# Kernel tuning notes

Measured on AMD Instinct MI355X. Metric: run time of the kernel, lower is better.

The kernel has to match this reference:

```python
import jax, jax.numpy as jnp
import numpy as np

B, Dx, Dz, Dy, H = 4096, 512, 512, 256, 2048
T0, T1 = 0.0, 1.0
N_STEPS = 64


def setup_inputs() -> dict:
    key = jax.random.key(0)
    ks = jax.random.split(key, 9)
    X = jax.random.normal(ks[0], (B, Dx), jnp.float32)
    # P sampled Uniform(0.01, 0.1) as in the torch module
    P = jax.random.uniform(ks[1], (Dz, Dx), jnp.float32, 0.01, 0.1)
    # A scaled so spectral radius ~1 -> exp(A*T) stays bounded over the integration
    A = jax.random.normal(ks[2], (Dz, Dz), jnp.float32) * (Dz ** -0.5)
    W1 = jax.random.normal(ks[3], (H, Dz), jnp.float32) * (Dz ** -0.5)
    b1 = jax.random.normal(ks[4], (H,), jnp.float32) * 0.01
    W2 = jax.random.normal(ks[5], (H, H), jnp.float32) * (H ** -0.5)
    b2 = jax.random.normal(ks[6], (H,), jnp.float32) * 0.01
    W3 = jax.random.normal(ks[7], (Dy, H), jnp.float32) * (H ** -0.5)
    b3 = jax.random.normal(ks[8], (Dy,), jnp.float32) * 0.01
    return dict(X=X, P=P, A=A, W1=W1, b1=b1, W2=W2, b2=b2, W3=W3, b3=b3,
                n_steps=N_STEPS)


def reference(X, P, A, W1, b1, W2, b2, W3, b3, n_steps):
    # Z0 = einsum('ji,bi->bj', P, X)  -> projection into latent ODE state
    z0 = X @ P.T  # [B, Dz]
    dt = jnp.float32((T1 - T0) / n_steps)

    def f(z):  # dz/dt = A z, batched: einsum('ji,bi->bj', A, z)
        return z @ A.T

    def rk4_step(z, _):
        k1 = f(z)
        k2 = f(z + 0.5 * dt * k1)
        k3 = f(z + 0.5 * dt * k2)
        k4 = f(z + dt * k3)
        return z + (dt / 6.0) * (k1 + 2.0 * k2 + 2.0 * k3 + k4), None

    zT, _ = jax.lax.scan(rk4_step, z0, None, length=n_steps)  # [B, Dz]

    # QnnMatrixODE MLP head (n_layers=3): Lin+ReLU, Lin+ReLU, Lin
    h = jax.nn.relu(zT @ W1.T + b1)
    h = jax.nn.relu(h @ W2.T + b2)
    y = h @ W3.T + b3  # [B, Dy]
    return y
```

## Files before the change

kernel.cpp:

```cpp
#include <hip/hip_runtime.h>

#define BDIM 4096
#define DX 512
#define DZ 512
#define DY 256
#define HD 2048
#define NSTEPS 64
#define LDT 72

typedef __attribute__((ext_vector_type(8))) short bf16x8;
typedef __attribute__((ext_vector_type(4))) float f32x4;

__device__ inline unsigned short f2bf(float f) {
    unsigned u = __float_as_uint(f);
    unsigned r = 0x7FFFu + ((u >> 16) & 1u);
    return (unsigned short)((u + r) >> 16);
}
__device__ inline float bf2f(unsigned short h) {
    return __uint_as_float(((unsigned)h) << 16);
}

#define GLDS16(g, l)                                                            \
    __builtin_amdgcn_global_load_lds((const __attribute__((address_space(1))) void*)(g), \
                                     (__attribute__((address_space(3))) void*)(l), 16, 0, 0)

struct CvtJobs {
    const float* src[5];
    unsigned short* hi[5];
    unsigned short* lo[5];
    int n4[5];
};
__global__ __launch_bounds__(256) void cvt_multi_k(CvtJobs J) {
    const int j = blockIdx.y;
    const int i4 = blockIdx.x * 256 + threadIdx.x;
    if (i4 >= J.n4[j]) return;
    float4 v = ((const float4*)J.src[j])[i4];
    ushort4 h;
    h.x = f2bf(v.x); h.y = f2bf(v.y); h.z = f2bf(v.z); h.w = f2bf(v.w);
    ((ushort4*)J.hi[j])[i4] = h;
    if (J.lo[j]) {
        ushort4 l;
        l.x = f2bf(v.x - bf2f(h.x));
        l.y = f2bf(v.y - bf2f(h.y));
        l.z = f2bf(v.z - bf2f(h.z));
        l.w = f2bf(v.w - bf2f(h.w));
        ((ushort4*)J.lo[j])[i4] = l;
    }
}

__global__ __launch_bounds__(256) void split_t_k(const float* __restrict__ A0,
                                                 unsigned short* __restrict__ H0,
                                                 unsigned short* __restrict__ L0,
                                                 const float* __restrict__ A1,
                                                 unsigned short* __restrict__ H1,
                                                 unsigned short* __restrict__ L1, int D) {
    const float* A = blockIdx.z ? A1 : A0;
    unsigned short* HT = blockIdx.z ? H1 : H0;
    unsigned short* LT = blockIdx.z ? L1 : L0;
    __shared__ float t[32][33];
    const int bx = blockIdx.x * 32, by = blockIdx.y * 32;
    const int x = threadIdx.x, y = threadIdx.y;
#pragma unroll
    for (int dy = 0; dy < 32; dy += 8)
        t[y + dy][x] = A[(size_t)(by + y + dy) * D + bx + x];
    __syncthreads();
#pragma unroll
    for (int dy = 0; dy < 32; dy += 8) {
        float v = t[x][y + dy];
        unsigned short h = f2bf(v);
        size_t o = (size_t)(bx + y + dy) * D + by + x;
        HT[o] = h;
        LT[o] = f2bf(v - bf2f(h));
    }
}

__global__ __launch_bounds__(256) void taylor_t_k(const float* __restrict__ Am,
                                                  const float* __restrict__ M2f,
                                                  const float* __restrict__ M3f,
                                                  const float* __restrict__ M4f,
                                                  unsigned short* __restrict__ Sh,
                                                  unsigned short* __restrict__ Sl,
                                                  unsigned short* __restrict__ STh,
                                                  unsigned short* __restrict__ STl,
                                                  int D, float h) {
    __shared__ float t[32][33];
    const float c2 = 0.5f * h * h;
    const float c3 = h * h * h * (1.0f / 6.0f);
    const float c4 = h * h * h * h * (1.0f / 24.0f);
    const int bx = blockIdx.x * 32, by = blockIdx.y * 32;
    const int x = threadIdx.x, y = threadIdx.y;
#pragma unroll
    for (int dy = 0; dy < 32; dy += 8) {
        const int row = by + y + dy, col = bx + x;
        const size_t idx = (size_t)row * D + col;
        float s = h * Am[idx] + c2 * M2f[idx] + c3 * M3f[idx] + c4 * M4f[idx];
        if (row == col) s += 1.0f;
        t[y + dy][x] = s;
        unsigned short hi = f2bf(s);
        Sh[idx] = hi;
        Sl[idx] = f2bf(s - bf2f(hi));
    }
    __syncthreads();
#pragma unroll
    for (int dy = 0; dy < 32; dy += 8) {
        float s = t[x][y + dy];
        size_t o = (size_t)(bx + y + dy) * D + by + x;
        unsigned short hi = f2bf(s);
        STh[o] = hi;
        STl[o] = f2bf(s - bf2f(hi));
    }
}

struct G64In { const unsigned short *Ahi, *Alo, *Bhi, *Blo; };
struct G64Out { float* Cf32; unsigned short *Chi, *Clo, *CThi, *CTlo; };

__device__ __forceinline__ void g64_core(int bx, int by, int M, int N, int K,
                                         G64In in, G64Out o,
                                         unsigned short* Ash, unsigned short* Asl,
                                         unsigned short* Bsh, unsigned short* Bsl) {
    const int tid = threadIdx.x;
    const int lane = tid & 63;
    const int wave = tid >> 6;
    const int wr = wave >> 1, wc = wave & 1;
    const int row0 = by * 64, col0 = bx * 64;
    const int sr = tid >> 2;
    const int sk = (tid & 3) * 16;

    const int niter = K >> 6;
    bf16x8 pa0, pa1, pl0, pl1, pb0, pb1, pq0, pq1;
    {
        const unsigned short* ar = in.Ahi + (size_t)(row0 + sr) * K + sk;
        const unsigned short* al = in.Alo + (size_t)(row0 + sr) * K + sk;
        const unsigned short* br = in.Bhi + (size_t)(col0 + sr) * K + sk;
        const unsigned short* bl = in.Blo + (size_t)(col0 + sr) * K + sk;
        pa0 = *(const bf16x8*)ar; pa1 = *(const bf16x8*)(ar + 8);
        pl0 = *(const bf16x8*)al; pl1 = *(const bf16x8*)(al + 8);
        pb0 = *(const bf16x8*)br; pb1 = *(const bf16x8*)(br + 8);
        pq0 = *(const bf16x8*)bl; pq1 = *(const bf16x8*)(bl + 8);
    }

    f32x4 acc[4] = {};
    const int mb = wr * 32 + (lane & 15);
    const int nb = wc * 32 + (lane & 15);

    for (int it = 0; it < niter; ++it) {
        __syncthreads();
        *(bf16x8*)&Ash[sr * LDT + sk] = pa0; *(bf16x8*)&Ash[sr * LDT + sk + 8] = pa1;
        *(bf16x8*)&Asl[sr * LDT + sk] = pl0; *(bf16x8*)&Asl[sr * LDT + sk + 8] = pl1;
        *(bf16x8*)&Bsh[sr * LDT + sk] = pb0; *(bf16x8*)&Bsh[sr * LDT + sk + 8] = pb1;
        *(bf16x8*)&Bsl[sr * LDT + sk] = pq0; *(bf16x8*)&Bsl[sr * LDT + sk + 8] = pq1;
        __syncthreads();

        {
            const int kn = (it + 1 < niter) ? ((it + 1) << 6) : 0;
            const unsigned short* ar = in.Ahi + (size_t)(row0 + sr) * K + kn + sk;
            const unsigned short* al = in.Alo + (size_t)(row0 + sr) * K + kn + sk;
            const unsigned short* br = in.Bhi + (size_t)(col0 + sr) * K + kn + sk;
            const unsigned short* bl = in.Blo + (size_t)(col0 + sr) * K + kn + sk;
            pa0 = *(const bf16x8*)ar; pa1 = *(const bf16x8*)(ar + 8);
            pl0 = *(const bf16x8*)al; pl1 = *(const bf16x8*)(al + 8);
            pb0 = *(const bf16x8*)br; pb1 = *(const bf16x8*)(br + 8);
            pq0 = *(const bf16x8*)bl; pq1 = *(const bf16x8*)(bl + 8);
        }

#pragma unroll
        for (int kh = 0; kh < 2; ++kh) {
            const int kk = kh * 32 + (lane >> 4) * 8;
            bf16x8 ah[2], alx[2], bh[2], blx[2];
#pragma unroll
            for (int t = 0; t < 2; ++t) {
                ah[t]  = *(const bf16x8*)&Ash[(mb + t * 16) * LDT + kk];
                alx[t] = *(const bf16x8*)&Asl[(mb + t * 16) * LDT + kk];
                bh[t]  = *(const bf16x8*)&Bsh[(nb + t * 16) * LDT + kk];
                blx[t] = *(const bf16x8*)&Bsl[(nb + t * 16) * LDT + kk];
            }
#pragma unroll
            for (int mt = 0; mt < 2; ++mt)
#pragma unroll
                for (int nt = 0; nt < 2; ++nt) {
                    acc[mt * 2 + nt] = __builtin_amdgcn_mfma_f32_16x16x32_bf16(
                        ah[mt], bh[nt], acc[mt * 2 + nt], 0, 0, 0);
                    acc[mt * 2 + nt] = __builtin_amdgcn_mfma_f32_16x16x32_bf16(
                        ah[mt], blx[nt], acc[mt * 2 + nt], 0, 0, 0);
                    acc[mt * 2 + nt] = __builtin_amdgcn_mfma_f32_16x16x32_bf16(
                        alx[mt], bh[nt], acc[mt * 2 + nt], 0, 0, 0);
                }
        }
    }

#pragma unroll
    for (int mt = 0; mt < 2; ++mt) {
        const int grow = row0 + wr * 32 + mt * 16 + (lane >> 4) * 4;
#pragma unroll
        for (int nt = 0; nt < 2; ++nt) {
            const int gcol = col0 + wc * 32 + nt * 16 + (lane & 15);
            f32x4 a = acc[mt * 2 + nt];
            unsigned short h4[4], l4[4];
#pragma unroll
            for (int i = 0; i < 4; ++i) {
                h4[i] = f2bf(a[i]);
                l4[i] = f2bf(a[i] - bf2f(h4[i]));
            }
            if (o.Cf32) {
#pragma unroll
                for (int i = 0; i < 4; ++i) o.Cf32[(size_t)(grow + i) * N + gcol] = a[i];
            }
            if (o.Chi) {
#pragma unroll
                for (int i = 0; i < 4; ++i) o.Chi[(size_t)(grow + i) * N + gcol] = h4[i];
            }
            if (o.Clo) {
#pragma unroll
                for (int i = 0; i < 4; ++i) o.Clo[(size_t)(grow + i) * N + gcol] = l4[i];
            }
            if (o.CThi) {
                ushort4 u = {h4[0], h4[1], h4[2], h4[3]};
                *(ushort4*)&o.CThi[(size_t)gcol * M + grow] = u;
            }
            if (o.CTlo) {
                ushort4 u = {l4[0], l4[1], l4[2], l4[3]};
                *(ushort4*)&o.CTlo[(size_t)gcol * M + grow] = u;
            }
        }
    }
}

__global__ __launch_bounds__(256) void g64_one(G64In in, G64Out o, int M, int N, int K) {
    __shared__ unsigned short Ash[64 * LDT], Asl[64 * LDT], Bsh[64 * LDT], Bsl[64 * LDT];
    g64_core(blockIdx.x, blockIdx.y, M, N, K, in, o, Ash, Asl, Bsh, Bsl);
}

__global__ __launch_bounds__(256) void g64_dual(G64In i0, G64Out o0, G64In i1, G64Out o1,
                                                int M, int N, int K) {
    __shared__ unsigned short Ash[64 * LDT], Asl[64 * LDT], Bsh[64 * LDT], Bsl[64 * LDT];
    g64_core(blockIdx.x, blockIdx.y, M, N, K, blockIdx.z ? i1 : i0, blockIdx.z ? o1 : o0,
             Ash, Asl, Bsh, Bsl);
}

template <int RELU, int BIAS, int OUT_BF16>
__global__ __launch_bounds__(256) void gemm_bf16(int M, int N, int K,
                                                 const unsigned short* __restrict__ A,
                                                 const unsigned short* __restrict__ B,
                                                 void* __restrict__ C,
                                                 const float* __restrict__ bias) {
    __shared__ unsigned short As[128 * 32];
    __shared__ unsigned short Bs[128 * 32];

    const int tid = threadIdx.x;
    const int lane = tid & 63;
    const int wave = tid >> 6;
    const int wr = wave >> 1, wc = wave & 1;
    const int row0 = blockIdx.y * 128;
    const int col0 = blockIdx.x * 128;

    const int srow = lane >> 2;
    const int schunk = (lane & 3) * 8;

    f32x4 acc[4][4] = {};

    for (int k0 = 0; k0 < K; k0 += 32) {
        const int r0 = wave * 32;
        GLDS16(A + (size_t)(row0 + r0 + srow) * K + k0 + schunk, &As[r0 * 32]);
        GLDS16(A + (size_t)(row0 + r0 + 16 + srow) * K + k0 + schunk, &As[(r0 + 16) * 32]);
        GLDS16(B + (size_t)(col0 + r0 + srow) * K + k0 + schunk, &Bs[r0 * 32]);
        GLDS16(B + (size_t)(col0 + r0 + 16 + srow) * K + k0 + schunk, &Bs[(r0 + 16) * 32]);
        __syncthreads();

        const int kk = (lane >> 4) * 8;
        const int mbase = wr * 64 + (lane & 15);
        const int nbase = wc * 64 + (lane & 15);
        bf16x8 af[4], bf[4];
#pragma unroll
        for (int t = 0; t < 4; ++t) {
            af[t] = *(const bf16x8*)&As[(mbase + t * 16) * 32 + kk];
            bf[t] = *(const bf16x8*)&Bs[(nbase + t * 16) * 32 + kk];
        }
#pragma unroll
        for (int mt = 0; mt < 4; ++mt)
#pragma unroll
            for (int nt = 0; nt < 4; ++nt)
                acc[mt][nt] = __builtin_amdgcn_mfma_f32_16x16x32_bf16(af[mt], bf[nt],
                                                                      acc[mt][nt], 0, 0, 0);
        __syncthreads();
    }

#pragma unroll
    for (int mt = 0; mt < 4; ++mt) {
        const int grow = row0 + wr * 64 + mt * 16 + (lane >> 4) * 4;
#pragma unroll
        for (int nt = 0; nt < 4; ++nt) {
            const int gcol = col0 + wc * 64 + nt * 16 + (lane & 15);
            const float bv = BIAS ? bias[gcol] : 0.0f;
#pragma unroll
            for (int i = 0; i < 4; ++i) {
                float v = acc[mt][nt][i] + bv;
                if (RELU) v = fmaxf(v, 0.0f);
                const size_t off = (size_t)(grow + i) * N + gcol;
                if (OUT_BF16)
                    ((unsigned short*)C)[off] = f2bf(v);
                else
                    ((float*)C)[off] = v;
            }
        }
    }
}

__global__ __launch_bounds__(256) void gemm64nt_f32(int M, int N, int K,
                                                    const unsigned short* __restrict__ A,
                                                    const unsigned short* __restrict__ B,
                                                    float* __restrict__ C,
                                                    const float* __restrict__ bias) {
    __shared__ unsigned short As[64 * 32];
    __shared__ unsigned short Bs[64 * 32];
    const int tid = threadIdx.x;
    const int lane = tid & 63;
    const int wave = tid >> 6;
    const int wr = wave >> 1, wc = wave & 1;
    const int row0 = blockIdx.y * 64;
    const int col0 = blockIdx.x * 64;
    const int r = tid >> 2, kq = (tid & 3) * 8;

    f32x4 acc[4] = {};

    for (int k0 = 0; k0 < K; k0 += 32) {
        bf16x8 av = *(const bf16x8*)(A + (size_t)(row0 + r) * K + k0 + kq);
        bf16x8 bv = *(const bf16x8*)(B + (size_t)(col0 + r) * K + k0 + kq);
        __syncthreads();
        *(bf16x8*)&As[r * 32 + kq] = av;
        *(bf16x8*)&Bs[r * 32 + kq] = bv;
        __syncthreads();

        const int kk = (lane >> 4) * 8;
        const int mb = wr * 32 + (lane & 15);
        const int nb = wc * 32 + (lane & 15);
        bf16x8 af[2], bf[2];
#pragma unroll
        for (int t = 0; t < 2; ++t) {
            af[t] = *(const bf16x8*)&As[(mb + t * 16) * 32 + kk];
            bf[t] = *(const bf16x8*)&Bs[(nb + t * 16) * 32 + kk];
        }
#pragma unroll
        for (int mt = 0; mt < 2; ++mt)
#pragma unroll
            for (int nt = 0; nt < 2; ++nt)
                acc[mt * 2 + nt] = __builtin_amdgcn_mfma_f32_16x16x32_bf16(
                    af[mt], bf[nt], acc[mt * 2 + nt], 0, 0, 0);
    }

#pragma unroll
    for (int mt = 0; mt < 2; ++mt) {
        const int grow = row0 + wr * 32 + mt * 16 + (lane >> 4) * 4;
#pragma unroll
        for (int nt = 0; nt < 2; ++nt) {
            const int gcol = col0 + wc * 32 + nt * 16 + (lane & 15);
            const float bv = bias ? bias[gcol] : 0.0f;
#pragma unroll
            for (int i = 0; i < 4; ++i)
                C[(size_t)(grow + i) * N + gcol] = acc[mt * 2 + nt][i] + bv;
        }
    }
}

extern "C" void kernel_launch(void* const* d_in, const int* in_sizes, int n_in,
                              void* d_out, int out_size, void* d_ws, size_t ws_size,
                              hipStream_t stream) {
    const float* X  = (const float*)d_in[0];
    const float* P  = (const float*)d_in[1];
    const float* Am = (const float*)d_in[2];
    const float* W1 = (const float*)d_in[3];
    const float* b1 = (const float*)d_in[4];
    const float* W2 = (const float*)d_in[5];
    const float* b2 = (const float*)d_in[6];
    const float* W3 = (const float*)d_in[7];
    const float* b3 = (const float*)d_in[8];
    float* out = (float*)d_out;

    const float h = 1.0f / (float)NSTEPS;
    const size_t S = (size_t)DZ * DZ;

    char* p = (char*)d_ws;
    auto alloc_f = [&](size_t n) { float* r = (float*)p; p += n * 4; return r; };
    auto alloc_h = [&](size_t n) { unsigned short* r = (unsigned short*)p; p += ((n * 2 + 15) & ~15ull); return r; };
    unsigned short* Xb   = alloc_h((size_t)BDIM * DX);
    unsigned short* W2b  = alloc_h((size_t)HD * HD);
    unsigned short* W3b  = alloc_h((size_t)DY * HD);
    unsigned short* W1h  = alloc_h((size_t)HD * DZ);
    unsigned short* W1l  = alloc_h((size_t)HD * DZ);
    unsigned short* Ah   = alloc_h(S);
    unsigned short* Al   = alloc_h(S);
    unsigned short* ATh  = alloc_h(S);
    unsigned short* ATl  = alloc_h(S);
    unsigned short* PTh  = alloc_h(S);
    unsigned short* PTl  = alloc_h(S);
    float* M2f = alloc_f(S);
    float* M3f = alloc_f(S);
    float* M4f = alloc_f(S);
    unsigned short* M2h  = alloc_h(S);
    unsigned short* M2l  = alloc_h(S);
    unsigned short* M2Th = alloc_h(S);
    unsigned short* M2Tl = alloc_h(S);
    unsigned short* Shb[2]  = {alloc_h(S), alloc_h(S)};
    unsigned short* Slb[2]  = {alloc_h(S), alloc_h(S)};
    unsigned short* SThb[2] = {alloc_h(S), alloc_h(S)};
    unsigned short* STlb[2] = {alloc_h(S), alloc_h(S)};
    unsigned short* RTh  = alloc_h(S);
    unsigned short* RTl  = alloc_h(S);
    unsigned short* C1b  = alloc_h((size_t)HD * DZ);
    unsigned short* h1b  = alloc_h((size_t)BDIM * HD);
    unsigned short* h2b  = alloc_h((size_t)BDIM * HD);

    CvtJobs J;
    J.src[0] = X;  J.hi[0] = Xb;  J.lo[0] = nullptr; J.n4[0] = BDIM * DX / 4;
    J.src[1] = W2; J.hi[1] = W2b; J.lo[1] = nullptr; J.n4[1] = HD * HD / 4;
    J.src[2] = W3; J.hi[2] = W3b; J.lo[2] = nullptr; J.n4[2] = DY * HD / 4;
    J.src[3] = W1; J.hi[3] = W1h; J.lo[3] = W1l;     J.n4[3] = HD * DZ / 4;
    J.src[4] = Am; J.hi[4] = Ah;  J.lo[4] = Al;      J.n4[4] = (int)(S / 4);
    cvt_multi_k<<<dim3(HD * HD / 4 / 256, 5), 256, 0, stream>>>(J);

    split_t_k<<<dim3(DZ / 32, DZ / 32, 2), dim3(32, 8), 0, stream>>>(
        Am, ATh, ATl, P, PTh, PTl, DZ);

    dim3 g8(DZ / 64, DZ / 64);
    const G64Out ONULL = {nullptr, nullptr, nullptr, nullptr, nullptr};

    {
        G64In i{Ah, Al, ATh, ATl};
        G64Out o{M2f, M2h, M2l, M2Th, M2Tl};
        g64_one<<<g8, 256, 0, stream>>>(i, o, DZ, DZ, DZ);
    }
    {
        G64In i0{M2h, M2l, ATh, ATl};
        G64Out o0 = ONULL; o0.Cf32 = M3f;
        G64In i1{M2h, M2l, M2Th, M2Tl};
        G64Out o1 = ONULL; o1.Cf32 = M4f;
        g64_dual<<<dim3(DZ / 64, DZ / 64, 2), 256, 0, stream>>>(i0, o0, i1, o1, DZ, DZ, DZ);
    }
    taylor_t_k<<<dim3(DZ / 32, DZ / 32), dim3(32, 8), 0, stream>>>(
        Am, M2f, M3f, M4f, Shb[0], Slb[0], SThb[0], STlb[0], DZ, h);
    int cur = 0;
    for (int s = 0; s < 6; ++s) {
        G64In i{Shb[cur], Slb[cur], SThb[cur], STlb[cur]};
        G64Out o{nullptr, Shb[1 - cur], Slb[1 - cur], SThb[1 - cur], STlb[1 - cur]};
        g64_one<<<g8, 256, 0, stream>>>(i, o, DZ, DZ, DZ);
        cur ^= 1;
    }
    {
        G64In i{Shb[cur], Slb[cur], PTh, PTl};
        G64Out o = ONULL; o.CThi = RTh; o.CTlo = RTl;
        g64_one<<<g8, 256, 0, stream>>>(i, o, DZ, DZ, DZ);
    }
    {
        G64In i{W1h, W1l, RTh, RTl};
        G64Out o = ONULL; o.Chi = C1b;
        g64_one<<<dim3(DZ / 64, HD / 64), 256, 0, stream>>>(i, o, HD, DZ, DZ);
    }

    gemm_bf16<1, 1, 1><<<dim3(HD / 128, BDIM / 128), 256, 0, stream>>>(
        BDIM, HD, DX, Xb, C1b, h1b, b1);
    gemm_bf16<1, 1, 1><<<dim3(HD / 128, BDIM / 128), 256, 0, stream>>>(
        BDIM, HD, HD, h1b, W2b, h2b, b2);
    gemm64nt_f32<<<dim3(DY / 64, BDIM / 64), 256, 0, stream>>>(
        BDIM, DY, HD, h2b, W3b, out, b3);
}
```

Before: 303.4 us.

## Compute exp(A) via Horner Taylor series and retile the MLP GEMMs

The matrix exponential is no longer built as an RK4 step matrix raised to the 64th power by six squarings. It is now a degree-15 Taylor series of exp(A) evaluated in Horner form on A^4, with the low-order polynomial blocks formed in one elementwise kernel and added in the GEMM epilogue. This replaces the Taylor build and six squarings with three Horner GEMMs, so there are fewer dependent 512x512 launches. The MLP GEMMs change as well: the first two use 64x128 tiles, which doubles the block count, and the last layer gets a double-buffered K=64 loop with register prefetch and padded LDS. The exact exponential differs slightly from the RK4 result, within its truncation error.

```diff
diff --git a/kernel.cpp b/kernel.cpp
--- a/kernel.cpp
+++ b/kernel.cpp
@@ -5,7 +5,6 @@
 #define DZ 512
 #define DY 256
 #define HD 2048
-#define NSTEPS 64
 #define LDT 72
 
 typedef __attribute__((ext_vector_type(8))) short bf16x8;
@@ -74,44 +73,50 @@
     }
 }
 
-__global__ __launch_bounds__(256) void taylor_t_k(const float* __restrict__ Am,
-                                                  const float* __restrict__ M2f,
-                                                  const float* __restrict__ M3f,
-                                                  const float* __restrict__ M4f,
-                                                  unsigned short* __restrict__ Sh,
-                                                  unsigned short* __restrict__ Sl,
-                                                  unsigned short* __restrict__ STh,
-                                                  unsigned short* __restrict__ STl,
-                                                  int D, float h) {
-    __shared__ float t[32][33];
-    const float c2 = 0.5f * h * h;
-    const float c3 = h * h * h * (1.0f / 6.0f);
-    const float c4 = h * h * h * h * (1.0f / 24.0f);
-    const int bx = blockIdx.x * 32, by = blockIdx.y * 32;
-    const int x = threadIdx.x, y = threadIdx.y;
-#pragma unroll
-    for (int dy = 0; dy < 32; dy += 8) {
-        const int row = by + y + dy, col = bx + x;
-        const size_t idx = (size_t)row * D + col;
-        float s = h * Am[idx] + c2 * M2f[idx] + c3 * M3f[idx] + c4 * M4f[idx];
-        if (row == col) s += 1.0f;
-        t[y + dy][x] = s;
-        unsigned short hi = f2bf(s);
-        Sh[idx] = hi;
-        Sl[idx] = f2bf(s - bf2f(hi));
-    }
-    __syncthreads();
-#pragma unroll
-    for (int dy = 0; dy < 32; dy += 8) {
-        float s = t[x][y + dy];
-        size_t o = (size_t)(bx + y + dy) * D + by + x;
-        unsigned short hi = f2bf(s);
-        STh[o] = hi;
-        STl[o] = f2bf(s - bf2f(hi));
-    }
-}
-
-struct G64In { const unsigned short *Ahi, *Alo, *Bhi, *Blo; };
+__global__ __launch_bounds__(256) void e0_k(const float* __restrict__ A,
+                                            const float* __restrict__ A2,
+                                            const float* __restrict__ A3,
+                                            float* __restrict__ B0,
+                                            float* __restrict__ B1,
+                                            float* __restrict__ B2,
+                                            unsigned short* __restrict__ B3h,
+                                            unsigned short* __restrict__ B3l) {
+    const int i4 = blockIdx.x * 256 + threadIdx.x;
+    const int base = i4 * 4;
+    const int row = base >> 9, col = base & 511;
+    const int d = row - col;
+    float4 a = ((const float4*)A)[i4];
+    float4 a2 = ((const float4*)A2)[i4];
+    float4 a3 = ((const float4*)A3)[i4];
+    float av[4] = {a.x, a.y, a.z, a.w};
+    float a2v[4] = {a2.x, a2.y, a2.z, a2.w};
+    float a3v[4] = {a3.x, a3.y, a3.z, a3.w};
+    float b0[4], b1[4], b2[4];
+    ushort4 h3, l3;
+    unsigned short* h3p = &h3.x;
+    unsigned short* l3p = &l3.x;
+#pragma unroll
+    for (int j = 0; j < 4; ++j) {
+        const float di = (j == d) ? 1.0f : 0.0f;
+        b0[j] = di + av[j] + 0.5f * a2v[j] + 1.6666667e-1f * a3v[j];
+        b1[j] = 4.1666668e-2f * di + 8.3333333e-3f * av[j] +
+                1.3888889e-3f * a2v[j] + 1.9841270e-4f * a3v[j];
+        b2[j] = 2.4801587e-5f * di + 2.7557319e-6f * av[j] +
+                2.7557319e-7f * a2v[j] + 2.5052108e-8f * a3v[j];
+        float b3 = 2.0876757e-9f * di + 1.6059044e-10f * av[j] +
+                   1.1470746e-11f * a2v[j] + 7.6471637e-13f * a3v[j];
+        unsigned short hh = f2bf(b3);
+        h3p[j] = hh;
+        l3p[j] = f2bf(b3 - bf2f(hh));
+    }
+    ((float4*)B0)[i4] = make_float4(b0[0], b0[1], b0[2], b0[3]);
+    ((float4*)B1)[i4] = make_float4(b1[0], b1[1], b1[2], b1[3]);
+    ((float4*)B2)[i4] = make_float4(b2[0], b2[1], b2[2], b2[3]);
+    ((ushort4*)B3h)[i4] = h3;
+    ((ushort4*)B3l)[i4] = l3;
+}
+
+struct G64In { const unsigned short *Ahi, *Alo, *Bhi, *Blo; const float* Dadd; };
 struct G64Out { float* Cf32; unsigned short *Chi, *Clo, *CThi, *CTlo; };
 
 __device__ __forceinline__ void g64_core(int bx, int by, int M, int N, int K,
@@ -195,6 +200,11 @@
         for (int nt = 0; nt < 2; ++nt) {
             const int gcol = col0 + wc * 32 + nt * 16 + (lane & 15);
             f32x4 a = acc[mt * 2 + nt];
+            if (in.Dadd) {
+#pragma unroll
+                for (int i = 0; i < 4; ++i)
+                    a[i] += in.Dadd[(size_t)(grow + i) * N + gcol];
+            }
             unsigned short h4[4], l4[4];
 #pragma unroll
             for (int i = 0; i < 4; ++i) {
@@ -226,57 +236,57 @@
 }
 
 __global__ __launch_bounds__(256) void g64_one(G64In in, G64Out o, int M, int N, int K) {
-    __shared__ unsigned short Ash[64 * LDT], Asl[64 * LDT], Bsh[64 * LDT], Bsl[64 * LDT];
+    __shared__ __align__(16) unsigned short Ash[64 * LDT], Asl[64 * LDT];
+    __shared__ __align__(16) unsigned short Bsh[64 * LDT], Bsl[64 * LDT];
     g64_core(blockIdx.x, blockIdx.y, M, N, K, in, o, Ash, Asl, Bsh, Bsl);
 }
 
 __global__ __launch_bounds__(256) void g64_dual(G64In i0, G64Out o0, G64In i1, G64Out o1,
                                                 int M, int N, int K) {
-    __shared__ unsigned short Ash[64 * LDT], Asl[64 * LDT], Bsh[64 * LDT], Bsl[64 * LDT];
+    __shared__ __align__(16) unsigned short Ash[64 * LDT], Asl[64 * LDT];
+    __shared__ __align__(16) unsigned short Bsh[64 * LDT], Bsl[64 * LDT];
     g64_core(blockIdx.x, blockIdx.y, M, N, K, blockIdx.z ? i1 : i0, blockIdx.z ? o1 : o0,
              Ash, Asl, Bsh, Bsl);
 }
 
 template <int RELU, int BIAS, int OUT_BF16>
-__global__ __launch_bounds__(256) void gemm_bf16(int M, int N, int K,
-                                                 const unsigned short* __restrict__ A,
-                                                 const unsigned short* __restrict__ B,
-                                                 void* __restrict__ C,
-                                                 const float* __restrict__ bias) {
-    __shared__ unsigned short As[128 * 32];
+__global__ __launch_bounds__(256) void gemm_bf16_v2(int M, int N, int K,
+                                                    const unsigned short* __restrict__ A,
+                                                    const unsigned short* __restrict__ B,
+                                                    void* __restrict__ C,
+                                                    const float* __restrict__ bias) {
+    __shared__ unsigned short As[64 * 32];
     __shared__ unsigned short Bs[128 * 32];
 
     const int tid = threadIdx.x;
     const int lane = tid & 63;
     const int wave = tid >> 6;
     const int wr = wave >> 1, wc = wave & 1;
-    const int row0 = blockIdx.y * 128;
+    const int row0 = blockIdx.y * 64;
     const int col0 = blockIdx.x * 128;
 
     const int srow = lane >> 2;
     const int schunk = (lane & 3) * 8;
 
-    f32x4 acc[4][4] = {};
+    f32x4 acc[2][4] = {};
 
     for (int k0 = 0; k0 < K; k0 += 32) {
-        const int r0 = wave * 32;
-        GLDS16(A + (size_t)(row0 + r0 + srow) * K + k0 + schunk, &As[r0 * 32]);
-        GLDS16(A + (size_t)(row0 + r0 + 16 + srow) * K + k0 + schunk, &As[(r0 + 16) * 32]);
-        GLDS16(B + (size_t)(col0 + r0 + srow) * K + k0 + schunk, &Bs[r0 * 32]);
-        GLDS16(B + (size_t)(col0 + r0 + 16 + srow) * K + k0 + schunk, &Bs[(r0 + 16) * 32]);
+        GLDS16(A + (size_t)(row0 + wave * 16 + srow) * K + k0 + schunk, &As[(wave * 16) * 32]);
+        GLDS16(B + (size_t)(col0 + wave * 32 + srow) * K + k0 + schunk, &Bs[(wave * 32) * 32]);
+        GLDS16(B + (size_t)(col0 + wave * 32 + 16 + srow) * K + k0 + schunk,
+               &Bs[(wave * 32 + 16) * 32]);
         __syncthreads();
 
         const int kk = (lane >> 4) * 8;
-        const int mbase = wr * 64 + (lane & 15);
+        const int mbase = wr * 32 + (lane & 15);
         const int nbase = wc * 64 + (lane & 15);
-        bf16x8 af[4], bf[4];
-#pragma unroll
-        for (int t = 0; t < 4; ++t) {
-            af[t] = *(const bf16x8*)&As[(mbase + t * 16) * 32 + kk];
-            bf[t] = *(const bf16x8*)&Bs[(nbase + t * 16) * 32 + kk];
-        }
-#pragma unroll
-        for (int mt = 0; mt < 4; ++mt)
+        bf16x8 af[2], bf[4];
+#pragma unroll
+        for (int t = 0; t < 2; ++t) af[t] = *(const bf16x8*)&As[(mbase + t * 16) * 32 + kk];
+#pragma unroll
+        for (int t = 0; t < 4; ++t) bf[t] = *(const bf16x8*)&Bs[(nbase + t * 16) * 32 + kk];
+#pragma unroll
+        for (int mt = 0; mt < 2; ++mt)
 #pragma unroll
             for (int nt = 0; nt < 4; ++nt)
                 acc[mt][nt] = __builtin_amdgcn_mfma_f32_16x16x32_bf16(af[mt], bf[nt],
@@ -285,8 +295,8 @@
     }
 
 #pragma unroll
-    for (int mt = 0; mt < 4; ++mt) {
-        const int grow = row0 + wr * 64 + mt * 16 + (lane >> 4) * 4;
+    for (int mt = 0; mt < 2; ++mt) {
+        const int grow = row0 + wr * 32 + mt * 16 + (lane >> 4) * 4;
 #pragma unroll
         for (int nt = 0; nt < 4; ++nt) {
             const int gcol = col0 + wc * 64 + nt * 16 + (lane & 15);
@@ -305,46 +315,64 @@
     }
 }
 
-__global__ __launch_bounds__(256) void gemm64nt_f32(int M, int N, int K,
-                                                    const unsigned short* __restrict__ A,
-                                                    const unsigned short* __restrict__ B,
-                                                    float* __restrict__ C,
-                                                    const float* __restrict__ bias) {
-    __shared__ unsigned short As[64 * 32];
-    __shared__ unsigned short Bs[64 * 32];
+__global__ __launch_bounds__(256) void gemm64nt_y(int M, int N, int K,
+                                                  const unsigned short* __restrict__ A,
+                                                  const unsigned short* __restrict__ B,
+                                                  float* __restrict__ C,
+                                                  const float* __restrict__ bias) {
+    __shared__ __align__(16) unsigned short As[64 * LDT];
+    __shared__ __align__(16) unsigned short Bs[64 * LDT];
     const int tid = threadIdx.x;
     const int lane = tid & 63;
     const int wave = tid >> 6;
     const int wr = wave >> 1, wc = wave & 1;
     const int row0 = blockIdx.y * 64;
     const int col0 = blockIdx.x * 64;
-    const int r = tid >> 2, kq = (tid & 3) * 8;
+    const int sr = tid >> 2, sk = (tid & 3) * 16;
+
+    const int niter = K >> 6;
+    bf16x8 pa0, pa1, pb0, pb1;
+    {
+        const unsigned short* ar = A + (size_t)(row0 + sr) * K + sk;
+        const unsigned short* br = B + (size_t)(col0 + sr) * K + sk;
+        pa0 = *(const bf16x8*)ar; pa1 = *(const bf16x8*)(ar + 8);
+        pb0 = *(const bf16x8*)br; pb1 = *(const bf16x8*)(br + 8);
+    }
 
     f32x4 acc[4] = {};
-
-    for (int k0 = 0; k0 < K; k0 += 32) {
-        bf16x8 av = *(const bf16x8*)(A + (size_t)(row0 + r) * K + k0 + kq);
-        bf16x8 bv = *(const bf16x8*)(B + (size_t)(col0 + r) * K + k0 + kq);
+    const int mb = wr * 32 + (lane & 15);
+    const int nb = wc * 32 + (lane & 15);
+
+    for (int it = 0; it < niter; ++it) {
         __syncthreads();
-        *(bf16x8*)&As[r * 32 + kq] = av;
-        *(bf16x8*)&Bs[r * 32 + kq] = bv;
+        *(bf16x8*)&As[sr * LDT + sk] = pa0; *(bf16x8*)&As[sr * LDT + sk + 8] = pa1;
+        *(bf16x8*)&Bs[sr * LDT + sk] = pb0; *(bf16x8*)&Bs[sr * LDT + sk + 8] = pb1;
         __syncthreads();
 
-        const int kk = (lane >> 4) * 8;
-        const int mb = wr * 32 + (lane & 15);
-        const int nb = wc * 32 + (lane & 15);
-        bf16x8 af[2], bf[2];
-#pragma unroll
-        for (int t = 0; t < 2; ++t) {
-            af[t] = *(const bf16x8*)&As[(mb + t * 16) * 32 + kk];
-            bf[t] = *(const bf16x8*)&Bs[(nb + t * 16) * 32 + kk];
-        }
-#pragma unroll
-        for (int mt = 0; mt < 2; ++mt)
-#pragma unroll
-            for (int nt = 0; nt < 2; ++nt)
-                acc[mt * 2 + nt] = __builtin_amdgcn_mfma_f32_16x16x32_bf16(
-                    af[mt], bf[nt], acc[mt * 2 + nt], 0, 0, 0);
+        {
+            const int kn = (it + 1 < niter) ? ((it + 1) << 6) : 0;
+            const unsigned short* ar = A + (size_t)(row0 + sr) * K + kn + sk;
+            const unsigned short* br = B + (size_t)(col0 + sr) * K + kn + sk;
+            pa0 = *(const bf16x8*)ar; pa1 = *(const bf16x8*)(ar + 8);
+            pb0 = *(const bf16x8*)br; pb1 = *(const bf16x8*)(br + 8);
+        }
+
+#pragma unroll
+        for (int kh = 0; kh < 2; ++kh) {
+            const int kk = kh * 32 + (lane >> 4) * 8;
+            bf16x8 af[2], bf[2];
+#pragma unroll
+            for (int t = 0; t < 2; ++t) {
+                af[t] = *(const bf16x8*)&As[(mb + t * 16) * LDT + kk];
+                bf[t] = *(const bf16x8*)&Bs[(nb + t * 16) * LDT + kk];
+            }
+#pragma unroll
+            for (int mt = 0; mt < 2; ++mt)
+#pragma unroll
+                for (int nt = 0; nt < 2; ++nt)
+                    acc[mt * 2 + nt] = __builtin_amdgcn_mfma_f32_16x16x32_bf16(
+                        af[mt], bf[nt], acc[mt * 2 + nt], 0, 0, 0);
+        }
     }
 
 #pragma unroll
@@ -375,7 +403,6 @@
     const float* b3 = (const float*)d_in[8];
     float* out = (float*)d_out;
 
-    const float h = 1.0f / (float)NSTEPS;
     const size_t S = (size_t)DZ * DZ;
 
     char* p = (char*)d_ws;
@@ -392,17 +419,25 @@
     unsigned short* ATl  = alloc_h(S);
     unsigned short* PTh  = alloc_h(S);
     unsigned short* PTl  = alloc_h(S);
-    float* M2f = alloc_f(S);
-    float* M3f = alloc_f(S);
-    float* M4f = alloc_f(S);
-    unsigned short* M2h  = alloc_h(S);
-    unsigned short* M2l  = alloc_h(S);
-    unsigned short* M2Th = alloc_h(S);
-    unsigned short* M2Tl = alloc_h(S);
-    unsigned short* Shb[2]  = {alloc_h(S), alloc_h(S)};
-    unsigned short* Slb[2]  = {alloc_h(S), alloc_h(S)};
-    unsigned short* SThb[2] = {alloc_h(S), alloc_h(S)};
-    unsigned short* STlb[2] = {alloc_h(S), alloc_h(S)};
+    float* A2f = alloc_f(S);
+    float* A3f = alloc_f(S);
+    unsigned short* A2h  = alloc_h(S);
+    unsigned short* A2l  = alloc_h(S);
+    unsigned short* A2Th = alloc_h(S);
+    unsigned short* A2Tl = alloc_h(S);
+    unsigned short* A4Th = alloc_h(S);
+    unsigned short* A4Tl = alloc_h(S);
+    float* B0f = alloc_f(S);
+    float* B1f = alloc_f(S);
+    float* B2f = alloc_f(S);
+    unsigned short* B3h  = alloc_h(S);
+    unsigned short* B3l  = alloc_h(S);
+    unsigned short* H1h  = alloc_h(S);
+    unsigned short* H1l  = alloc_h(S);
+    unsigned short* H2h  = alloc_h(S);
+    unsigned short* H2l  = alloc_h(S);
+    unsigned short* H3h  = alloc_h(S);
+    unsigned short* H3l  = alloc_h(S);
     unsigned short* RTh  = alloc_h(S);
     unsigned short* RTl  = alloc_h(S);
     unsigned short* C1b  = alloc_h((size_t)HD * DZ);
@@ -421,44 +456,51 @@
         Am, ATh, ATl, P, PTh, PTl, DZ);
 
     dim3 g8(DZ / 64, DZ / 64);
-    const G64Out ONULL = {nullptr, nullptr, nullptr, nullptr, nullptr};
-
-    {
-        G64In i{Ah, Al, ATh, ATl};
-        G64Out o{M2f, M2h, M2l, M2Th, M2Tl};
+
+    {
+        G64In i{Ah, Al, ATh, ATl, nullptr};
+        G64Out o{A2f, A2h, A2l, A2Th, A2Tl};
         g64_one<<<g8, 256, 0, stream>>>(i, o, DZ, DZ, DZ);
     }
     {
-        G64In i0{M2h, M2l, ATh, ATl};
-        G64Out o0 = ONULL; o0.Cf32 = M3f;
-        G64In i1{M2h, M2l, M2Th, M2Tl};
-        G64Out o1 = ONULL; o1.Cf32 = M4f;
+        G64In i0{A2h, A2l, ATh, ATl, nullptr};
+        G64Out o0{A3f, nullptr, nullptr, nullptr, nullptr};
+        G64In i1{A2h, A2l, A2Th, A2Tl, nullptr};
+        G64Out o1{nullptr, nullptr, nullptr, A4Th, A4Tl};
         g64_dual<<<dim3(DZ / 64, DZ / 64, 2), 256, 0, stream>>>(i0, o0, i1, o1, DZ, DZ, DZ);
     }
-    taylor_t_k<<<dim3(DZ / 32, DZ / 32), dim3(32, 8), 0, stream>>>(
-        Am, M2f, M3f, M4f, Shb[0], Slb[0], SThb[0], STlb[0], DZ, h);
-    int cur = 0;
-    for (int s = 0; s < 6; ++s) {
-        G64In i{Shb[cur], Slb[cur], SThb[cur], STlb[cur]};
-        G64Out o{nullptr, Shb[1 - cur], Slb[1 - cur], SThb[1 - cur], STlb[1 - cur]};
+    e0_k<<<dim3((int)(S / 4 / 256)), 256, 0, stream>>>(Am, A2f, A3f, B0f, B1f, B2f, B3h, B3l);
+
+    {
+        G64In i{B3h, B3l, A4Th, A4Tl, B2f};
+        G64Out o{nullptr, H1h, H1l, nullptr, nullptr};
         g64_one<<<g8, 256, 0, stream>>>(i, o, DZ, DZ, DZ);
-        cur ^= 1;
-    }
-    {
-        G64In i{Shb[cur], Slb[cur], PTh, PTl};
-        G64Out o = ONULL; o.CThi = RTh; o.CTlo = RTl;
+    }
+    {
+        G64In i{H1h, H1l, A4Th, A4Tl, B1f};
+        G64Out o{nullptr, H2h, H2l, nullptr, nullptr};
         g64_one<<<g8, 256, 0, stream>>>(i, o, DZ, DZ, DZ);
     }
     {
-        G64In i{W1h, W1l, RTh, RTl};
-        G64Out o = ONULL; o.Chi = C1b;
+        G64In i{H2h, H2l, A4Th, A4Tl, B0f};
+        G64Out o{nullptr, H3h, H3l, nullptr, nullptr};
+        g64_one<<<g8, 256, 0, stream>>>(i, o, DZ, DZ, DZ);
+    }
+    {
+        G64In i{H3h, H3l, PTh, PTl, nullptr};
+        G64Out o{nullptr, nullptr, nullptr, RTh, RTl};
+        g64_one<<<g8, 256, 0, stream>>>(i, o, DZ, DZ, DZ);
+    }
+    {
+        G64In i{W1h, W1l, RTh, RTl, nullptr};
+        G64Out o{nullptr, C1b, nullptr, nullptr, nullptr};
         g64_one<<<dim3(DZ / 64, HD / 64), 256, 0, stream>>>(i, o, HD, DZ, DZ);
     }
 
-    gemm_bf16<1, 1, 1><<<dim3(HD / 128, BDIM / 128), 256, 0, stream>>>(
+    gemm_bf16_v2<1, 1, 1><<<dim3(HD / 128, BDIM / 64), 256, 0, stream>>>(
         BDIM, HD, DX, Xb, C1b, h1b, b1);
-    gemm_bf16<1, 1, 1><<<dim3(HD / 128, BDIM / 128), 256, 0, stream>>>(
+    gemm_bf16_v2<1, 1, 1><<<dim3(HD / 128, BDIM / 64), 256, 0, stream>>>(
         BDIM, HD, HD, h1b, W2b, h2b, b2);
-    gemm64nt_f32<<<dim3(DY / 64, BDIM / 64), 256, 0, stream>>>(
+    gemm64nt_y<<<dim3(DY / 64, BDIM / 64), 256, 0, stream>>>(
         BDIM, DY, HD, h2b, W3b, out, b3);
 }
```

After: 267.3 us. 11.9% less time.
